# Kernel tuning notes

Hardware: AMD Instinct MI355X
Metric: run time of the kernel (lower is better)

## Reference

```python
import jax, jax.numpy as jnp
import numpy as np

SMOOTHING = 0.1
IGNORE_INDEX = 0


def setup_inputs() -> dict:
    key = jax.random.key(0)
    k1, k2 = jax.random.split(key)
    B, L, V = 4, 2048, 32000
    # probabilities (module takes probs and applies torch.log itself);
    # normalize uniform draws over vocab so rows are valid prob distributions
    p = jax.random.uniform(k1, (B, L, V), dtype=jnp.float32, minval=1e-3, maxval=1.0)
    p = p / p.sum(axis=-1, keepdims=True)
    targets = jax.random.randint(k2, (B, L), 0, V, dtype=jnp.int64 if jax.config.jax_enable_x64 else jnp.int32)
    return {"inputs": p, "targets": targets, "norm": B * L}


def reference(inputs, targets, norm):
    # KLDiv(log p, q) with q = onehot*(1-s) + s/V, summed over vocab,
    # masked where targets == ignore_index, summed and divided by norm.
    # sum_v q_v*(log q_v - log p_v) computed without materializing the one-hot:
    V = inputs.shape[-1]
    s = SMOOTHING
    a = s / V                 # off-target prob
    b = 1.0 - s + a           # on-target prob
    logp = jnp.log(inputs)                                   # [B,L,V]
    logp_t = jnp.take_along_axis(logp, targets[..., None], axis=-1)[..., 0]  # [B,L]
    sum_logp = logp.sum(axis=-1)                             # [B,L]
    const = a * np.log(a) * (V - 1) + b * np.log(b)          # entropy-like constant
    loss = const - a * (sum_logp - logp_t) - b * logp_t      # [B,L]
    loss = jnp.where(targets == IGNORE_INDEX, 0.0, loss)
    return loss.sum() / norm
```

## Files before the change

kernel.cpp:

```cpp
#include <hip/hip_runtime.h>
#include <cmath>


template<int NV4>
__global__ __launch_bounds__(256) void ls_row_kernel(
    const float* __restrict__ p,
    const int*   __restrict__ tgt,
    const int*   __restrict__ normp,
    float*       __restrict__ out,
    float cterm, int V, int nv4_rt)
{
    const int row = blockIdx.x;
    const int tid = threadIdx.x;
    const int t   = tgt[row];
    if (t == 0) return;

    const float*  prow = p + (size_t)row * (size_t)V;
    const float4* p4   = (const float4*)prow;
    const int     nv4  = (NV4 > 0) ? NV4 : nv4_rt;

    float s0 = 0.f, s1 = 0.f, s2 = 0.f, s3 = 0.f;
    #pragma unroll 4
    for (int i = tid; i < nv4; i += 256) {
        float4 v = p4[i];
        s0 += __logf(v.x);
        s1 += __logf(v.y);
        s2 += __logf(v.z);
        s3 += __logf(v.w);
    }
    float s = (s0 + s1) + (s2 + s3);

    #pragma unroll
    for (int off = 32; off > 0; off >>= 1)
        s += __shfl_down(s, off, 64);

    __shared__ float wsum[4];
    const int wid  = tid >> 6;
    const int lane = tid & 63;
    if (lane == 0) wsum[wid] = s;
    __syncthreads();

    if (tid == 0) {
        float tot = (wsum[0] + wsum[1]) + (wsum[2] + wsum[3]);
        float lt  = __logf(prow[t]);

        const float a = 0.1f / (float)V;
        const float b = 1.0f - 0.1f + a;
        float loss = cterm - a * (tot - lt) - b * lt;

        int   ni = normp[0];
        float nf = (ni > 0 && ni < (1 << 30)) ? (float)ni : __int_as_float(ni);

        atomicAdd(out, loss / nf);
    }
}

extern "C" void kernel_launch(void* const* d_in, const int* in_sizes, int n_in,
                              void* d_out, int out_size, void* d_ws, size_t ws_size,
                              hipStream_t stream) {
    const float* p     = (const float*)d_in[0];
    const int*   tgt   = (const int*)d_in[1];
    const int*   normp = (const int*)d_in[2];
    float*       out   = (float*)d_out;

    const int BL = in_sizes[1];
    const int V  = in_sizes[0] / in_sizes[1];

    const double a = 0.1 / (double)V;
    const double b = 1.0 - 0.1 + a;
    const float  cterm = (float)(a * log(a) * (double)(V - 1) + b * log(b));

    hipMemsetAsync(d_out, 0, sizeof(float), stream);

    if (V == 32000) {
        ls_row_kernel<8000><<<BL, 256, 0, stream>>>(p, tgt, normp, out, cterm, V, 0);
    } else {
        ls_row_kernel<0><<<BL, 256, 0, stream>>>(p, tgt, normp, out, cterm, V, V >> 2);
    }
}
```

Baseline: 1.289 ms.

## Flatten log-sum over whole tensor, subtract masked rows, finalize with two-stage reduction

Rewrites the loss algebraically so the sum of log-probabilities is computed over the entire flat tensor by a fixed grid of 2048 blocks with grid-stride loops. Per-row target terms and a correction for ignored rows are computed separately, and one final kernel reduces both partial arrays in double precision. This replaces the per-row launch, which had one block per row plus an atomic add per row. The goal is better load balance and streaming bandwidth. In exchange it adds two extra launches and work that scales with the number of masked rows, which are re-read to cancel their contribution.

```diff
diff --git a/kernel.cpp b/kernel.cpp
--- a/kernel.cpp
+++ b/kernel.cpp
@@ -1,6 +1,119 @@
 #include <hip/hip_runtime.h>
 #include <cmath>
 
+
+#define LS_LN2 0.6931471805599453094172321214581766
+
+template<int N4C, int STRIDE_C>
+__global__ __launch_bounds__(256) void ls_flat_log2sum(
+    const float* __restrict__ p,
+    float*       __restrict__ partA,
+    int n4_rt)
+{
+    const int n4     = (N4C      > 0) ? N4C      : n4_rt;
+    const int stride = (STRIDE_C > 0) ? STRIDE_C : (int)(gridDim.x * blockDim.x);
+    const float4* __restrict__ p4 = (const float4*)p;
+
+    float s0 = 0.f, s1 = 0.f, s2 = 0.f, s3 = 0.f;
+    #pragma unroll 5
+    for (int i = blockIdx.x * 256 + threadIdx.x; i < n4; i += stride) {
+        float4 v = p4[i];
+        s0 += __log2f(v.x);
+        s1 += __log2f(v.y);
+        s2 += __log2f(v.z);
+        s3 += __log2f(v.w);
+    }
+    float s = (s0 + s1) + (s2 + s3);
+
+    #pragma unroll
+    for (int off = 32; off > 0; off >>= 1)
+        s += __shfl_down(s, off, 64);
+
+    __shared__ float wsum[4];
+    const int wid  = threadIdx.x >> 6;
+    const int lane = threadIdx.x & 63;
+    if (lane == 0) wsum[wid] = s;
+    __syncthreads();
+    if (threadIdx.x == 0)
+        partA[blockIdx.x] = (wsum[0] + wsum[1]) + (wsum[2] + wsum[3]);
+}
+
+__global__ __launch_bounds__(256) void ls_row_terms(
+    const float* __restrict__ p,
+    const int*   __restrict__ tgt,
+    float*       __restrict__ partB,
+    float cterm, float bma, float a_ln2,
+    int BL, int V)
+{
+    __shared__ int   masked[256];
+    __shared__ int   nmaskS;
+    __shared__ float wsum[4];
+    if (threadIdx.x == 0) nmaskS = 0;
+    __syncthreads();
+
+    const int r = blockIdx.x * 256 + threadIdx.x;
+    float my = 0.f;
+    if (r < BL) {
+        const int t = tgt[r];
+        if (t != 0) {
+            my = cterm - bma * __logf(p[(size_t)r * V + t]);
+        } else {
+            masked[atomicAdd(&nmaskS, 1)] = r;
+        }
+    }
+    __syncthreads();
+
+    const int nm = nmaskS;
+    for (int m = 0; m < nm; ++m) {
+        const int row = masked[m];
+        const float4* p4 = (const float4*)(p + (size_t)row * V);
+        float s = 0.f;
+        for (int i = threadIdx.x; i < (V >> 2); i += 256) {
+            float4 v = p4[i];
+            s += __log2f(v.x) + __log2f(v.y) + __log2f(v.z) + __log2f(v.w);
+        }
+        my += a_ln2 * s;
+    }
+
+    #pragma unroll
+    for (int off = 32; off > 0; off >>= 1)
+        my += __shfl_down(my, off, 64);
+    const int wid  = threadIdx.x >> 6;
+    const int lane = threadIdx.x & 63;
+    if (lane == 0) wsum[wid] = my;
+    __syncthreads();
+    if (threadIdx.x == 0)
+        partB[blockIdx.x] = (wsum[0] + wsum[1]) + (wsum[2] + wsum[3]);
+}
+
+__global__ __launch_bounds__(256) void ls_reduce_finalize(
+    const float* __restrict__ partA, int nA, float neg_a_ln2,
+    const float* __restrict__ partB, int nB,
+    const int*   __restrict__ normp,
+    float*       __restrict__ out)
+{
+    double s = 0.0;
+    for (int i = threadIdx.x; i < nA; i += 256)
+        s += (double)neg_a_ln2 * (double)partA[i];
+    for (int i = threadIdx.x; i < nB; i += 256)
+        s += (double)partB[i];
+
+    #pragma unroll
+    for (int off = 32; off > 0; off >>= 1)
+        s += __shfl_down(s, off, 64);
+
+    __shared__ double wsum[4];
+    const int wid  = threadIdx.x >> 6;
+    const int lane = threadIdx.x & 63;
+    if (lane == 0) wsum[wid] = s;
+    __syncthreads();
+    if (threadIdx.x == 0) {
+        double tot = ((wsum[0] + wsum[1]) + (wsum[2] + wsum[3]));
+        const int   ni = normp[0];
+        const float nf = (ni > 0 && ni < (1 << 30)) ? (float)ni : __int_as_float(ni);
+        out[0] = (float)(tot / (double)nf);
+    }
+}
 
 template<int NV4>
 __global__ __launch_bounds__(256) void ls_row_kernel(
@@ -29,7 +142,6 @@
         s3 += __logf(v.w);
     }
     float s = (s0 + s1) + (s2 + s3);
-
     #pragma unroll
     for (int off = 32; off > 0; off >>= 1)
         s += __shfl_down(s, off, 64);
@@ -43,14 +155,11 @@
     if (tid == 0) {
         float tot = (wsum[0] + wsum[1]) + (wsum[2] + wsum[3]);
         float lt  = __logf(prow[t]);
-
         const float a = 0.1f / (float)V;
         const float b = 1.0f - 0.1f + a;
         float loss = cterm - a * (tot - lt) - b * lt;
-
         int   ni = normp[0];
         float nf = (ni > 0 && ni < (1 << 30)) ? (float)ni : __int_as_float(ni);
-
         atomicAdd(out, loss / nf);
     }
 }
@@ -68,13 +177,33 @@
 
     const double a = 0.1 / (double)V;
     const double b = 1.0 - 0.1 + a;
-    const float  cterm = (float)(a * log(a) * (double)(V - 1) + b * log(b));
-
-    hipMemsetAsync(d_out, 0, sizeof(float), stream);
-
-    if (V == 32000) {
-        ls_row_kernel<8000><<<BL, 256, 0, stream>>>(p, tgt, normp, out, cterm, V, 0);
+    const float  cterm     = (float)(a * log(a) * (double)(V - 1) + b * log(b));
+    const float  bma       = (float)(b - a);
+    const float  a_ln2     = (float)(a * LS_LN2);
+    const float  neg_a_ln2 = -a_ln2;
+
+    const int       NA   = 2048;
+    const int       NB   = (BL + 255) / 256;
+    const long long n4ll = (long long)BL * (long long)(V >> 2);
+    const size_t    need = (size_t)(NA + NB) * sizeof(float);
+
+    if ((V & 3) == 0 && ws_size >= need && n4ll < (1LL << 31)) {
+        float* partA = (float*)d_ws;
+        float* partB = partA + NA;
+
+        if (V == 32000 && BL == 8192) {
+            ls_flat_log2sum<65536000, 2048 * 256>
+                <<<NA, 256, 0, stream>>>(p, partA, 0);
+        } else {
+            ls_flat_log2sum<0, 0>
+                <<<NA, 256, 0, stream>>>(p, partA, (int)n4ll);
+        }
+        ls_row_terms<<<NB, 256, 0, stream>>>(
+            p, tgt, partB, cterm, bma, a_ln2, BL, V);
+        ls_reduce_finalize<<<1, 256, 0, stream>>>(
+            partA, NA, neg_a_ln2, partB, NB, normp, out);
     } else {
+        hipMemsetAsync(d_out, 0, sizeof(float), stream);
         ls_row_kernel<0><<<BL, 256, 0, stream>>>(p, tgt, normp, out, cterm, V, V >> 2);
     }
 }
```

Result: no change. 1.297 ms (+0.6%).
